# Performance work log

Hardware: AMD Instinct MI355X
Metric: run time of the kernel (lower is better)

## Reference

```python
import jax, jax.numpy as jnp
import numpy as np

B, T, C, H = 2, 2048, 1024, 16
DH = C // H
EPS = 1e-5


def _rotary(t_len, d_head):
    inv_freq = 1.0 / (10000.0 ** (jnp.arange(0, d_head, 2, dtype=jnp.float32) / d_head))
    t = jnp.arange(t_len, dtype=jnp.float32)
    freqs = t[:, None] * inv_freq[None, :]           # [T, dh/2]
    emb = jnp.concatenate([freqs, freqs], axis=-1)    # [T, dh]
    return jnp.cos(emb), jnp.sin(emb)


def _apply_rope(x, cos, sin):
    # x: [B,H,T,dh]; cos/sin: [T,dh]
    d = x.shape[-1]
    x1, x2 = x[..., : d // 2], x[..., d // 2 :]
    x_rot = jnp.concatenate([-x2, x1], axis=-1)
    return x * cos + x_rot * sin


def _decay_mask(t_len, n_head):
    gammas = 1.0 - 2.0 ** (-5.0 - jnp.arange(n_head, dtype=jnp.float32))  # [H]
    n = jnp.arange(t_len)[:, None]
    m = jnp.arange(t_len)[None, :]
    dist = n - m
    decay = gammas[:, None, None] ** jnp.maximum(dist, 0).astype(jnp.float32)
    return jnp.where(dist[None] >= 0, decay, 0.0)  # [H,T,T]


def setup_inputs() -> dict:
    key = jax.random.key(0)
    ks = jax.random.split(key, 7)
    s = 1.0 / np.sqrt(C)
    return {
        "x": jax.random.normal(ks[0], (B, T, C), dtype=jnp.float32),
        "Wq": jax.random.normal(ks[1], (C, C), dtype=jnp.float32) * s,
        "Wk": jax.random.normal(ks[2], (C, C), dtype=jnp.float32) * s,
        "Wv": jax.random.normal(ks[3], (C, C), dtype=jnp.float32) * s,
        "Wo": jax.random.normal(ks[4], (C, C), dtype=jnp.float32) * s,
        "gn_weight": jnp.ones((C,), dtype=jnp.float32),
        "gn_bias": jnp.zeros((C,), dtype=jnp.float32),
    }


def reference(x, Wq, Wk, Wv, Wo, gn_weight, gn_bias):
    b, t, c = x.shape
    # projections (torch Linear: y = x @ W.T), split heads -> [B,H,T,dh]
    def proj(W):
        return jnp.einsum("btc,oc->bto", x, W).reshape(b, t, H, DH).transpose(0, 2, 1, 3)
    q, k, v = proj(Wq), proj(Wk), proj(Wv)

    cos, sin = _rotary(t, DH)
    q = _apply_rope(q, cos, sin)
    k = _apply_rope(k, cos, sin)

    decay = _decay_mask(t, H)                          # [H,T,T]
    qk = jnp.einsum("bhtd,bhsd->bhts", q, k) * (1.0 / np.sqrt(DH))
    qk = qk * decay[None]
    out = jnp.einsum("bhts,bhsd->bhtd", qk, v)         # [B,H,T,dh]

    # GroupNorm with n_head groups over channels, per token
    out = out.transpose(0, 2, 1, 3)                    # [B,T,H,dh]
    mu = jnp.mean(out, axis=-1, keepdims=True)
    var = jnp.mean((out - mu) ** 2, axis=-1, keepdims=True)
    out = (out - mu) * jax.lax.rsqrt(var + EPS)
    out = out * gn_weight.reshape(H, DH) + gn_bias.reshape(H, DH)

    out = out.reshape(b, t, c)
    return jnp.einsum("btc,oc->bto", out, Wo)
```

## Files before the change

kernel.cpp:

```cpp
#include <hip/hip_runtime.h>
#include <stdint.h>

#define B_ 2
#define T_ 2048
#define C_ 1024
#define H_ 16
#define DH_ 64
#define M_ (B_*T_)

typedef short bhalf8 __attribute__((ext_vector_type(8)));
typedef float floatx4 __attribute__((ext_vector_type(4)));

__device__ __forceinline__ short f2bf(float f) {
  unsigned u = __float_as_uint(f);
  u += 0x7fffu + ((u >> 16) & 1u);
  return (short)(u >> 16);
}
__device__ __forceinline__ float bf2f(short s) {
  return __uint_as_float(((unsigned)(unsigned short)s) << 16);
}

__device__ __forceinline__ void gll16(void* lds_dst, const void* g_src) {
  __builtin_amdgcn_global_load_lds(
      reinterpret_cast<const uint32_t __attribute__((address_space(1)))*>(
          reinterpret_cast<uintptr_t>(g_src)),
      reinterpret_cast<uint32_t __attribute__((address_space(3)))*>(
          reinterpret_cast<uintptr_t>(lds_dst)),
      16, 0, 0);
}

__global__ void cvt_all(
    const float* __restrict__ x,  const float* __restrict__ wq,
    const float* __restrict__ wk, const float* __restrict__ wv,
    const float* __restrict__ wo,
    short* __restrict__ xb, short* __restrict__ wqb, short* __restrict__ wkb,
    short* __restrict__ wvb, short* __restrict__ wob)
{
  int i = blockIdx.x * blockDim.x + threadIdx.x;
  const float* s; short* d; int off;
  if (i < (M_*C_/4)) { s = x; d = xb; off = i; }
  else {
    int j = i - M_*C_/4;
    int w = j >> 18;
    off = j & ((1<<18) - 1);
    s = (w==0) ? wq : (w==1) ? wk : (w==2) ? wv : wo;
    d = (w==0) ? wqb : (w==1) ? wkb : (w==2) ? wvb : wob;
  }
  float4 v = ((const float4*)s)[off];
  short4 o;
  o.x = f2bf(v.x); o.y = f2bf(v.y); o.z = f2bf(v.z); o.w = f2bf(v.w);
  ((short4*)d)[off] = o;
}

__global__ __launch_bounds__(256) void gemm_qkv(
    const short* __restrict__ X,
    const short* __restrict__ Wq, const short* __restrict__ Wk, const short* __restrict__ Wv,
    short* __restrict__ Qb, short* __restrict__ Kb, short* __restrict__ Vt)
{
  __shared__ __align__(16) short As[128*64];
  __shared__ __align__(16) short Bs[128*64];
  const int tid  = threadIdx.x;
  const int lane = tid & 63;
  const int wv   = tid >> 6;
  const int l15  = lane & 15;
  const int quad = lane >> 4;
  const int wm   = (wv >> 1) << 6;
  const int wn   = (wv & 1) << 6;
  const int nx   = blockIdx.x;
  const int m0   = blockIdx.y << 7;
  const int K    = C_;

  const short *Ab, *Bb;
  int nloc, kind;
  if (nx < 8)       { kind = 0; nloc = nx << 7;        Ab = X  + (size_t)m0*K;   Bb = Wq + (size_t)nloc*K; }
  else if (nx < 16) { kind = 1; nloc = (nx - 8) << 7;  Ab = X  + (size_t)m0*K;   Bb = Wk + (size_t)nloc*K; }
  else              { kind = 2; nloc = (nx - 16) << 7; Ab = Wv + (size_t)nloc*K; Bb = X  + (size_t)m0*K;   }

  floatx4 acc[4][4] = {};

  for (int k0 = 0; k0 < K; k0 += 64) {
    __syncthreads();
#pragma unroll
    for (int i = 0; i < 4; ++i) {
      int c = (i<<8) + tid, r = c >> 3, g = (c & 7) ^ (r & 7);
      gll16(&As[((i<<8) + (wv<<6))*8], Ab + (size_t)r*K + k0 + (g<<3));
      gll16(&Bs[((i<<8) + (wv<<6))*8], Bb + (size_t)r*K + k0 + (g<<3));
    }
    __syncthreads();
#pragma unroll
    for (int ks = 0; ks < 2; ++ks) {
      bhalf8 af[4], bfr[4];
#pragma unroll
      for (int rt = 0; rt < 4; ++rt) {
        int row = wm + rt*16 + l15;
        af[rt] = *(const bhalf8*)&As[(row<<6) + ((((ks<<2)+quad) ^ (row&7))<<3)];
      }
#pragma unroll
      for (int ct = 0; ct < 4; ++ct) {
        int row = wn + ct*16 + l15;
        bfr[ct] = *(const bhalf8*)&Bs[(row<<6) + ((((ks<<2)+quad) ^ (row&7))<<3)];
      }
#pragma unroll
      for (int rt = 0; rt < 4; ++rt)
#pragma unroll
        for (int ct = 0; ct < 4; ++ct)
          acc[rt][ct] = __builtin_amdgcn_mfma_f32_16x16x32_bf16(af[rt], bfr[ct], acc[rt][ct], 0, 0, 0);
    }
  }

  if (kind < 2) {
    short* Cb = kind ? Kb : Qb;
    const int hh = (nloc + wn) >> 6;
#pragma unroll
    for (int rt = 0; rt < 4; ++rt)
#pragma unroll
      for (int r = 0; r < 4; ++r) {
        int n  = m0 + wm + rt*16 + quad*4 + r;
        int bb = n >> 11, t = n & (T_-1);
        size_t base = ((size_t)(bb*H_ + hh)*T_ + t)*DH_;
        float tf = (float)t;
#pragma unroll
        for (int ct = 0; ct < 2; ++ct) {
          int ii = ct*16 + l15;
          float ang = tf * exp2f((float)ii * (-0.4152410118609203f));
          float sn = __sinf(ang), cs = __cosf(ang);
          float xlo = acc[rt][ct][r], xhi = acc[rt][ct+2][r];
          Cb[base + ii]      = f2bf(xlo*cs - xhi*sn);
          Cb[base + ii + 32] = f2bf(xhi*cs + xlo*sn);
        }
      }
  } else {
#pragma unroll
    for (int rt = 0; rt < 4; ++rt)
#pragma unroll
      for (int r = 0; r < 4; ++r) {
        int o = nloc + wm + rt*16 + quad*4 + r;
#pragma unroll
        for (int ct = 0; ct < 4; ++ct) {
          int n  = m0 + wn + ct*16 + l15;
          int bb = n >> 11, t = n & (T_-1);
          Vt[(size_t)bb*(C_*T_) + (size_t)o*T_ + t] = f2bf(acc[rt][ct][r]);
        }
      }
  }
}

__global__ __launch_bounds__(256) void gemm_out(
    const short* __restrict__ A, const short* __restrict__ Bm, float* __restrict__ Cf)
{
  __shared__ __align__(16) short As[128*64];
  __shared__ __align__(16) short Bs[64*64];
  const int tid = threadIdx.x, lane = tid & 63, wv = tid >> 6;
  const int l15 = lane & 15, quad = lane >> 4;
  const int n0 = blockIdx.x << 6;
  const int m0 = blockIdx.y << 7;

  floatx4 acc[2][4] = {};
  const short* Ab = A  + (size_t)m0 * C_;
  const short* Bb = Bm + (size_t)n0 * C_;

  for (int k0 = 0; k0 < C_; k0 += 64) {
    __syncthreads();
#pragma unroll
    for (int i = 0; i < 4; ++i) {
      int c = (i<<8) + tid, r = c >> 3, g = (c & 7) ^ (r & 7);
      gll16(&As[((i<<8) + (wv<<6))*8], Ab + (size_t)r*C_ + k0 + (g<<3));
    }
#pragma unroll
    for (int i = 0; i < 2; ++i) {
      int c = (i<<8) + tid, r = c >> 3, g = (c & 7) ^ (r & 7);
      gll16(&Bs[((i<<8) + (wv<<6))*8], Bb + (size_t)r*C_ + k0 + (g<<3));
    }
    __syncthreads();
#pragma unroll
    for (int ks = 0; ks < 2; ++ks) {
      bhalf8 af[2], bfr[4];
#pragma unroll
      for (int rt = 0; rt < 2; ++rt) {
        int row = (wv<<5) + rt*16 + l15;
        af[rt] = *(const bhalf8*)&As[(row<<6) + ((((ks<<2)+quad) ^ (row&7))<<3)];
      }
#pragma unroll
      for (int ct = 0; ct < 4; ++ct) {
        int row = ct*16 + l15;
        bfr[ct] = *(const bhalf8*)&Bs[(row<<6) + ((((ks<<2)+quad) ^ (row&7))<<3)];
      }
#pragma unroll
      for (int rt = 0; rt < 2; ++rt)
#pragma unroll
        for (int ct = 0; ct < 4; ++ct)
          acc[rt][ct] = __builtin_amdgcn_mfma_f32_16x16x32_bf16(af[rt], bfr[ct], acc[rt][ct], 0, 0, 0);
    }
  }

#pragma unroll
  for (int rt = 0; rt < 2; ++rt)
#pragma unroll
    for (int r = 0; r < 4; ++r) {
      int n = m0 + (wv<<5) + rt*16 + quad*4 + r;
#pragma unroll
      for (int ct = 0; ct < 4; ++ct)
        Cf[(size_t)n * C_ + n0 + ct*16 + l15] = acc[rt][ct][r];
    }
}

__global__ __launch_bounds__(256) void transpose_k(
    const short* __restrict__ Kb, short* __restrict__ Kt)
{
  __shared__ short tile[64*66];
  const int idx = blockIdx.x, bh = idx >> 5, tc = idx & 31;
  const int t0 = tc << 6;
  const short* src = Kb + ((size_t)bh*T_ + t0) * DH_;
  int row = threadIdx.x >> 2, c0 = (threadIdx.x & 3) << 4;
  *(int4*)&tile[row*66 + c0]     = *(const int4*)&src[row*64 + c0];
  *(int4*)&tile[row*66 + c0 + 8] = *(const int4*)&src[row*64 + c0 + 8];
  __syncthreads();
  short* dst = Kt + (size_t)bh*DH_*T_;
  int d = threadIdx.x >> 2, k0 = (threadIdx.x & 3) << 4;
  short tmp[16];
#pragma unroll
  for (int i = 0; i < 16; ++i) tmp[i] = tile[(k0 + i)*66 + d];
  *(int4*)&dst[(size_t)d*T_ + t0 + k0]     = *(const int4*)&tmp[0];
  *(int4*)&dst[(size_t)d*T_ + t0 + k0 + 8] = *(const int4*)&tmp[8];
}

__global__ __launch_bounds__(256) void seg_state(
    const short* __restrict__ Kt, const short* __restrict__ Vt,
    short* __restrict__ Pseg)
{
  __shared__ __align__(16) short Ks[64*64];
  __shared__ __align__(16) short Vs[64*64];
  const int tid = threadIdx.x, lane = tid & 63, wv = tid >> 6;
  const int l15 = lane & 15, quad = lane >> 4;
  const int wrow = wv << 4;
  const int bh = blockIdx.x >> 2, p = blockIdx.x & 3;
  const int h = bh & 15;
  const float log2g = log2f(1.f - exp2f(-5.f - (float)h));
  const float g64 = exp2f(log2g * 64.f);

  float wgt[16];
#pragma unroll
  for (int ks = 0; ks < 2; ++ks)
#pragma unroll
    for (int i = 0; i < 8; ++i)
      wgt[ks*8 + i] = exp2f(log2g * (float)(64 - (ks*32 + (quad<<3) + i)));

  const short* Ktg = Kt + (size_t)bh*DH_*T_;
  const short* Vtg = Vt + (size_t)bh*DH_*T_;

  floatx4 acc[4] = {};
  for (int j = 0; j < 8; ++j) {
    const int m0 = ((p<<3) + j) << 6;
    __syncthreads();
#pragma unroll
    for (int i = 0; i < 2; ++i) {
      int slot = (i<<8) + tid;
      int r = slot >> 3, g = (slot & 7) ^ (r & 7);
      gll16(&Ks[((i<<8) + (wv<<6))*8], Ktg + (size_t)r*T_ + m0 + (g<<3));
      gll16(&Vs[((i<<8) + (wv<<6))*8], Vtg + (size_t)r*T_ + m0 + (g<<3));
    }
    __syncthreads();
#pragma unroll
    for (int ct = 0; ct < 4; ++ct)
#pragma unroll
      for (int r = 0; r < 4; ++r) acc[ct][r] *= g64;
#pragma unroll
    for (int ks = 0; ks < 2; ++ks) {
      int row = wrow + l15;
      bhalf8 va = *(const bhalf8*)&Vs[(row<<6) + ((((ks<<2)+quad) ^ (row&7))<<3)];
      bhalf8 aw;
#pragma unroll
      for (int i = 0; i < 8; ++i) aw[i] = f2bf(bf2f(va[i]) * wgt[ks*8 + i]);
      bhalf8 bk[4];
#pragma unroll
      for (int ct = 0; ct < 4; ++ct) {
        int kr = ct*16 + l15;
        bk[ct] = *(const bhalf8*)&Ks[(kr<<6) + ((((ks<<2)+quad) ^ (kr&7))<<3)];
      }
#pragma unroll
      for (int ct = 0; ct < 4; ++ct)
        acc[ct] = __builtin_amdgcn_mfma_f32_16x16x32_bf16(aw, bk[ct], acc[ct], 0, 0, 0);
    }
  }
  size_t base = (size_t)(bh*4 + p) * 2 * 4096;
#pragma unroll
  for (int ct = 0; ct < 4; ++ct)
#pragma unroll
    for (int r = 0; r < 4; ++r) {
      int e = wrow + (quad<<2) + r, d = ct*16 + l15;
      float x = acc[ct][r];
      short hi = f2bf(x);
      short lo = f2bf(x - bf2f(hi));
      Pseg[base + e*64 + d]        = hi;
      Pseg[base + 4096 + e*64 + d] = lo;
    }
}

__global__ __launch_bounds__(256) void retention_chunk(
    const short* __restrict__ Qb, const short* __restrict__ Kb,
    const short* __restrict__ Kt, const short* __restrict__ Vt,
    const short* __restrict__ Pseg,
    const float* __restrict__ gnw, const float* __restrict__ gnb,
    short* __restrict__ Xn)
{
  __shared__ __align__(16) short Vs[64*64];
  __shared__ __align__(16) short Kts[64*64];
  __shared__ __align__(16) short KSs[64*64];
  __shared__ __align__(16) short Sh[64*64];
  __shared__ __align__(16) short Sl[64*64];

  const int tid = threadIdx.x, lane = tid & 63, wv = tid >> 6;
  const int l15 = lane & 15, quad = lane >> 4;
  const int wrow = wv << 4;

  const int idx = blockIdx.x;
  const int bh = idx & 31;
  const int cc = idx >> 5;
  const int c  = ((cc & 7) << 2) | (cc >> 3);
  const int p = c >> 3, j = c & 7;
  const int b = bh >> 4, h = bh & 15;
  const int n0 = c << 6;

  const float log2g = log2f(1.f - exp2f(-5.f - (float)h));
  const float g64 = exp2f(log2g * 64.f);

  const short* Qg  = Qb + ((size_t)bh*T_ + n0 + wrow) * DH_;
  const short* Kg  = Kb + (size_t)bh*T_*DH_;
  const short* Ktg = Kt + (size_t)bh*DH_*T_;
  const short* Vtg = Vt + (size_t)bh*DH_*T_;

  bhalf8 aq[2];
#pragma unroll
  for (int ks = 0; ks < 2; ++ks)
    aq[ks] = *(const bhalf8*)(Qg + (size_t)l15*DH_ + ks*32 + quad*8);

  float rowf[4], colf0[4];
#pragma unroll
  for (int r = 0; r < 4; ++r)
    rowf[r] = exp2f(log2g * (float)(wrow + (quad<<2) + r)) * 0.125f;
#pragma unroll
  for (int ct = 0; ct < 4; ++ct)
    colf0[ct] = exp2f(-log2g * (float)(ct*16 + l15));

  const bool has_state = (c > 0);

  floatx4 st[4] = {};
  if (j > 0) {
    float wgt[16];
#pragma unroll
    for (int ks = 0; ks < 2; ++ks)
#pragma unroll
      for (int i = 0; i < 8; ++i)
        wgt[ks*8 + i] = exp2f(log2g * (float)(64 - (ks*32 + (quad<<3) + i)));
    for (int jp = 0; jp < j; ++jp) {
      if (log2g * (float)((j - 1 - jp) << 6) < -34.f) continue;
      const int m0 = ((p<<3) + jp) << 6;
      __syncthreads();
#pragma unroll
      for (int i = 0; i < 2; ++i) {
        int slot = (i<<8) + tid;
        int r = slot >> 3, g = (slot & 7) ^ (r & 7);
        gll16(&Kts[((i<<8) + (wv<<6))*8], Ktg + (size_t)r*T_ + m0 + (g<<3));
        gll16(&Vs[((i<<8) + (wv<<6))*8],  Vtg + (size_t)r*T_ + m0 + (g<<3));
      }
      __syncthreads();
#pragma unroll
      for (int ct = 0; ct < 4; ++ct)
#pragma unroll
        for (int r = 0; r < 4; ++r) st[ct][r] *= g64;
#pragma unroll
      for (int ks = 0; ks < 2; ++ks) {
        int row = wrow + l15;
        bhalf8 va = *(const bhalf8*)&Vs[(row<<6) + ((((ks<<2)+quad) ^ (row&7))<<3)];
        bhalf8 aw;
#pragma unroll
        for (int i = 0; i < 8; ++i) aw[i] = f2bf(bf2f(va[i]) * wgt[ks*8 + i]);
        bhalf8 bk[4];
#pragma unroll
        for (int ct = 0; ct < 4; ++ct) {
          int kr = ct*16 + l15;
          bk[ct] = *(const bhalf8*)&Kts[(kr<<6) + ((((ks<<2)+quad) ^ (kr&7))<<3)];
        }
#pragma unroll
        for (int ct = 0; ct < 4; ++ct)
          st[ct] = __builtin_amdgcn_mfma_f32_16x16x32_bf16(aw, bk[ct], st[ct], 0, 0, 0);
      }
    }
  }
  for (int pp = 0; pp < p; ++pp) {
    float wexp = log2g * (float)(n0 - ((pp + 1) << 9));
    if (wexp < -34.f) continue;
    float w = exp2f(wexp);
    const short* Pg = Pseg + (size_t)(bh*4 + pp) * 2 * 4096;
#pragma unroll
    for (int ct = 0; ct < 4; ++ct)
#pragma unroll
      for (int r = 0; r < 4; ++r) {
        int e = wrow + (quad<<2) + r, d = ct*16 + l15;
        st[ct][r] += w * (bf2f(Pg[e*64 + d]) + bf2f(Pg[4096 + e*64 + d]));
      }
  }
  if (has_state) {
#pragma unroll
    for (int ct = 0; ct < 4; ++ct)
#pragma unroll
      for (int r = 0; r < 4; ++r) {
        int e = wrow + (quad<<2) + r, d = ct*16 + l15;
        float x = st[ct][r];
        short hi = f2bf(x);
        short lo = f2bf(x - bf2f(hi));
        int addr = (e<<6) + ((((d>>3) ^ (e&7))<<3)) + (d&7);
        Sh[addr] = hi; Sl[addr] = lo;
      }
  }

  __syncthreads();
#pragma unroll
  for (int i = 0; i < 2; ++i) {
    int slot = (i<<8) + tid;
    int r = slot >> 3, g = (slot & 7) ^ (r & 7);
    gll16(&KSs[((i<<8) + (wv<<6))*8], Kg  + (size_t)(n0 + r)*DH_ + (g<<3));
    gll16(&Vs[((i<<8) + (wv<<6))*8],  Vtg + (size_t)r*T_ + n0 + (g<<3));
  }
  __syncthreads();

  floatx4 sacc[4] = {};
#pragma unroll
  for (int ks = 0; ks < 2; ++ks) {
    bhalf8 bk[4];
#pragma unroll
    for (int ct = 0; ct < 4; ++ct) {
      int row = ct*16 + l15;
      bk[ct] = *(const bhalf8*)&KSs[(row<<6) + ((((ks<<2)+quad) ^ (row&7))<<3)];
    }
#pragma unroll
    for (int ct = 0; ct < 4; ++ct)
      sacc[ct] = __builtin_amdgcn_mfma_f32_16x16x32_bf16(aq[ks], bk[ct], sacc[ct], 0, 0, 0);
  }
  __syncthreads();
#pragma unroll
  for (int ct = 0; ct < 4; ++ct) {
    float cf = colf0[ct];
    int colg = (ct<<1) + (l15>>3);
    int m = ct*16 + l15;
#pragma unroll
    for (int r = 0; r < 4; ++r) {
      int row = wrow + (quad<<2) + r;
      float v = (row >= m) ? sacc[ct][r] * (rowf[r] * cf) : 0.f;
      KSs[(row<<6) + ((colg ^ ((row>>1)&7))<<3) + (l15&7)] = f2bf(v);
    }
  }
  floatx4 oacc[4] = {};
#pragma unroll
  for (int ks = 0; ks < 2; ++ks) {
    int row = wrow + l15;
    bhalf8 as_ = *(const bhalf8*)&KSs[(row<<6) + ((((ks<<2)+quad) ^ ((row>>1)&7))<<3)];
    bhalf8 bv[4];
#pragma unroll
    for (int ct = 0; ct < 4; ++ct) {
      int vrow = ct*16 + l15;
      bv[ct] = *(const bhalf8*)&Vs[(vrow<<6) + ((((ks<<2)+quad) ^ (vrow&7))<<3)];
    }
#pragma unroll
    for (int ct = 0; ct < 4; ++ct)
      oacc[ct] = __builtin_amdgcn_mfma_f32_16x16x32_bf16(as_, bv[ct], oacc[ct], 0, 0, 0);
  }

  if (has_state) {
    floatx4 iacc[4] = {};
#pragma unroll
    for (int ks = 0; ks < 2; ++ks) {
      bhalf8 bhf[4], blf[4];
#pragma unroll
      for (int ct = 0; ct < 4; ++ct) {
        int er = ct*16 + l15;
        int ga = ((((ks<<2)+quad) ^ (er&7))<<3);
        bhf[ct] = *(const bhalf8*)&Sh[(er<<6) + ga];
        blf[ct] = *(const bhalf8*)&Sl[(er<<6) + ga];
      }
#pragma unroll
      for (int ct = 0; ct < 4; ++ct) {
        iacc[ct] = __builtin_amdgcn_mfma_f32_16x16x32_bf16(aq[ks], bhf[ct], iacc[ct], 0, 0, 0);
        iacc[ct] = __builtin_amdgcn_mfma_f32_16x16x32_bf16(aq[ks], blf[ct], iacc[ct], 0, 0, 0);
      }
    }
#pragma unroll
    for (int ct = 0; ct < 4; ++ct)
#pragma unroll
      for (int r = 0; r < 4; ++r)
        oacc[ct][r] += rowf[r] * iacc[ct][r];
  }

#pragma unroll
  for (int r = 0; r < 4; ++r) {
    float s1 = oacc[0][r] + oacc[1][r] + oacc[2][r] + oacc[3][r];
    float s2 = oacc[0][r]*oacc[0][r] + oacc[1][r]*oacc[1][r]
             + oacc[2][r]*oacc[2][r] + oacc[3][r]*oacc[3][r];
#pragma unroll
    for (int off = 1; off < 16; off <<= 1) {
      s1 += __shfl_xor(s1, off);
      s2 += __shfl_xor(s2, off);
    }
    float mean = s1 * (1.f/64.f);
    float var  = s2 * (1.f/64.f) - mean*mean;
    float rstd = rsqrtf(var + 1e-5f);
    int t = n0 + wrow + (quad<<2) + r;
    size_t obase = ((size_t)b*T_ + t)*C_ + h*DH_;
#pragma unroll
    for (int ct = 0; ct < 4; ++ct) {
      int d = ct*16 + l15;
      float y = (oacc[ct][r] - mean)*rstd*gnw[h*DH_ + d] + gnb[h*DH_ + d];
      Xn[obase + d] = f2bf(y);
    }
  }
}

extern "C" void kernel_launch(void* const* d_in, const int* in_sizes, int n_in,
                              void* d_out, int out_size, void* d_ws, size_t ws_size,
                              hipStream_t stream) {
  (void)in_sizes; (void)n_in; (void)out_size; (void)ws_size;
  const float* x   = (const float*)d_in[0];
  const float* Wq  = (const float*)d_in[1];
  const float* Wk  = (const float*)d_in[2];
  const float* Wv  = (const float*)d_in[3];
  const float* Wo  = (const float*)d_in[4];
  const float* gnw = (const float*)d_in[5];
  const float* gnb = (const float*)d_in[6];
  float* out = (float*)d_out;

  char* ws = (char*)d_ws;
  short* Xb   = (short*)(ws);
  short* Ktb  = (short*)(ws);
  short* Wqb  = (short*)(ws + (8u<<20));
  short* Pseg = (short*)(ws + (8u<<20));
  short* Wkb  = (short*)(ws + (10u<<20));
  short* Wvb  = (short*)(ws + (12u<<20));
  short* Wob  = (short*)(ws + (14u<<20));
  short* Qb   = (short*)(ws + (16u<<20));
  short* Kb   = (short*)(ws + (24u<<20));
  short* Vtw  = (short*)(ws + (32u<<20));
  short* Xn   = (short*)(ws + (40u<<20));

  cvt_all<<<(M_*C_/4 + 4*(C_*C_/4)) / 256, 256, 0, stream>>>(
      x, Wq, Wk, Wv, Wo, Xb, Wqb, Wkb, Wvb, Wob);

  gemm_qkv<<<dim3(24, 32), 256, 0, stream>>>(Xb, Wqb, Wkb, Wvb, Qb, Kb, Vtw);
  transpose_k<<<1024, 256, 0, stream>>>(Kb, Ktb);
  seg_state<<<128, 256, 0, stream>>>(Ktb, Vtw, Pseg);
  retention_chunk<<<1024, 256, 0, stream>>>(Qb, Kb, Ktb, Vtw, Pseg, gnw, gnb, Xn);
  gemm_out<<<dim3(16, 32), 256, 0, stream>>>(Xn, Wob, out);
}
```

Measured before the change: 183.6 us.

## Double-buffer GEMM and segment-state LDS loads; split segments into eight parts

Both GEMMs now use a 32-wide K slice with two LDS buffers, so the next slice's global-to-LDS load is issued before the MFMAs on the current slice. This removes one barrier per iteration and hides load latency. seg_state also double-buffers, and the segment count per head grows from 4 to 8, giving 256 blocks instead of 128. retention_chunk adds one more cross-segment state term per chunk in exchange for shorter intra-segment loops.

```diff
diff --git a/kernel.cpp b/kernel.cpp
--- a/kernel.cpp
+++ b/kernel.cpp
@@ -57,8 +57,8 @@
     const short* __restrict__ Wq, const short* __restrict__ Wk, const short* __restrict__ Wv,
     short* __restrict__ Qb, short* __restrict__ Kb, short* __restrict__ Vt)
 {
-  __shared__ __align__(16) short As[128*64];
-  __shared__ __align__(16) short Bs[128*64];
+  __shared__ __align__(16) short As[2][128*32];
+  __shared__ __align__(16) short Bs[2][128*32];
   const int tid  = threadIdx.x;
   const int lane = tid & 63;
   const int wv   = tid >> 6;
@@ -76,36 +76,39 @@
   else if (nx < 16) { kind = 1; nloc = (nx - 8) << 7;  Ab = X  + (size_t)m0*K;   Bb = Wk + (size_t)nloc*K; }
   else              { kind = 2; nloc = (nx - 16) << 7; Ab = Wv + (size_t)nloc*K; Bb = X  + (size_t)m0*K;   }
 
+  auto stage = [&](int buf, int k0) {
+#pragma unroll
+    for (int i = 0; i < 2; ++i) {
+      int pA = (i<<8) + tid;
+      int r = pA >> 2, go = (pA & 3) ^ ((r >> 1) & 3);
+      gll16(&As[buf][((i<<8) + (wv<<6))*8], Ab + (size_t)r*K + k0 + (go<<3));
+      gll16(&Bs[buf][((i<<8) + (wv<<6))*8], Bb + (size_t)r*K + k0 + (go<<3));
+    }
+  };
+
   floatx4 acc[4][4] = {};
-
-  for (int k0 = 0; k0 < K; k0 += 64) {
+  stage(0, 0);
+  int cur = 0;
+  for (int it = 0; it < 32; ++it) {
     __syncthreads();
-#pragma unroll
-    for (int i = 0; i < 4; ++i) {
-      int c = (i<<8) + tid, r = c >> 3, g = (c & 7) ^ (r & 7);
-      gll16(&As[((i<<8) + (wv<<6))*8], Ab + (size_t)r*K + k0 + (g<<3));
-      gll16(&Bs[((i<<8) + (wv<<6))*8], Bb + (size_t)r*K + k0 + (g<<3));
-    }
-    __syncthreads();
-#pragma unroll
-    for (int ks = 0; ks < 2; ++ks) {
-      bhalf8 af[4], bfr[4];
-#pragma unroll
-      for (int rt = 0; rt < 4; ++rt) {
-        int row = wm + rt*16 + l15;
-        af[rt] = *(const bhalf8*)&As[(row<<6) + ((((ks<<2)+quad) ^ (row&7))<<3)];
-      }
-#pragma unroll
-      for (int ct = 0; ct < 4; ++ct) {
-        int row = wn + ct*16 + l15;
-        bfr[ct] = *(const bhalf8*)&Bs[(row<<6) + ((((ks<<2)+quad) ^ (row&7))<<3)];
-      }
-#pragma unroll
-      for (int rt = 0; rt < 4; ++rt)
-#pragma unroll
-        for (int ct = 0; ct < 4; ++ct)
-          acc[rt][ct] = __builtin_amdgcn_mfma_f32_16x16x32_bf16(af[rt], bfr[ct], acc[rt][ct], 0, 0, 0);
-    }
+    if (it < 31) stage(cur ^ 1, (it + 1) << 5);
+    bhalf8 af[4], bfr[4];
+#pragma unroll
+    for (int rt = 0; rt < 4; ++rt) {
+      int row = wm + rt*16 + l15;
+      af[rt] = *(const bhalf8*)&As[cur][(row<<5) + ((quad ^ ((row>>1)&3))<<3)];
+    }
+#pragma unroll
+    for (int ct = 0; ct < 4; ++ct) {
+      int row = wn + ct*16 + l15;
+      bfr[ct] = *(const bhalf8*)&Bs[cur][(row<<5) + ((quad ^ ((row>>1)&3))<<3)];
+    }
+#pragma unroll
+    for (int rt = 0; rt < 4; ++rt)
+#pragma unroll
+      for (int ct = 0; ct < 4; ++ct)
+        acc[rt][ct] = __builtin_amdgcn_mfma_f32_16x16x32_bf16(af[rt], bfr[ct], acc[rt][ct], 0, 0, 0);
+    cur ^= 1;
   }
 
   if (kind < 2) {
@@ -148,49 +151,51 @@
 __global__ __launch_bounds__(256) void gemm_out(
     const short* __restrict__ A, const short* __restrict__ Bm, float* __restrict__ Cf)
 {
-  __shared__ __align__(16) short As[128*64];
-  __shared__ __align__(16) short Bs[64*64];
+  __shared__ __align__(16) short As[2][128*32];
+  __shared__ __align__(16) short Bs[2][64*32];
   const int tid = threadIdx.x, lane = tid & 63, wv = tid >> 6;
   const int l15 = lane & 15, quad = lane >> 4;
   const int n0 = blockIdx.x << 6;
   const int m0 = blockIdx.y << 7;
 
-  floatx4 acc[2][4] = {};
   const short* Ab = A  + (size_t)m0 * C_;
   const short* Bb = Bm + (size_t)n0 * C_;
 
-  for (int k0 = 0; k0 < C_; k0 += 64) {
+  auto stage = [&](int buf, int k0) {
+#pragma unroll
+    for (int i = 0; i < 2; ++i) {
+      int p = (i<<8) + tid, r = p >> 2, go = (p & 3) ^ ((r >> 1) & 3);
+      gll16(&As[buf][((i<<8) + (wv<<6))*8], Ab + (size_t)r*C_ + k0 + (go<<3));
+    }
+    {
+      int p = tid, r = p >> 2, go = (p & 3) ^ ((r >> 1) & 3);
+      gll16(&Bs[buf][(wv<<6)*8], Bb + (size_t)r*C_ + k0 + (go<<3));
+    }
+  };
+
+  floatx4 acc[2][4] = {};
+  stage(0, 0);
+  int cur = 0;
+  for (int it = 0; it < 32; ++it) {
     __syncthreads();
-#pragma unroll
-    for (int i = 0; i < 4; ++i) {
-      int c = (i<<8) + tid, r = c >> 3, g = (c & 7) ^ (r & 7);
-      gll16(&As[((i<<8) + (wv<<6))*8], Ab + (size_t)r*C_ + k0 + (g<<3));
-    }
-#pragma unroll
-    for (int i = 0; i < 2; ++i) {
-      int c = (i<<8) + tid, r = c >> 3, g = (c & 7) ^ (r & 7);
-      gll16(&Bs[((i<<8) + (wv<<6))*8], Bb + (size_t)r*C_ + k0 + (g<<3));
-    }
-    __syncthreads();
-#pragma unroll
-    for (int ks = 0; ks < 2; ++ks) {
-      bhalf8 af[2], bfr[4];
-#pragma unroll
-      for (int rt = 0; rt < 2; ++rt) {
-        int row = (wv<<5) + rt*16 + l15;
-        af[rt] = *(const bhalf8*)&As[(row<<6) + ((((ks<<2)+quad) ^ (row&7))<<3)];
-      }
-#pragma unroll
-      for (int ct = 0; ct < 4; ++ct) {
-        int row = ct*16 + l15;
-        bfr[ct] = *(const bhalf8*)&Bs[(row<<6) + ((((ks<<2)+quad) ^ (row&7))<<3)];
-      }
-#pragma unroll
-      for (int rt = 0; rt < 2; ++rt)
-#pragma unroll
-        for (int ct = 0; ct < 4; ++ct)
-          acc[rt][ct] = __builtin_amdgcn_mfma_f32_16x16x32_bf16(af[rt], bfr[ct], acc[rt][ct], 0, 0, 0);
-    }
+    if (it < 31) stage(cur ^ 1, (it + 1) << 5);
+    bhalf8 af[2], bfr[4];
+#pragma unroll
+    for (int rt = 0; rt < 2; ++rt) {
+      int row = (wv<<5) + rt*16 + l15;
+      af[rt] = *(const bhalf8*)&As[cur][(row<<5) + ((quad ^ ((row>>1)&3))<<3)];
+    }
+#pragma unroll
+    for (int ct = 0; ct < 4; ++ct) {
+      int row = ct*16 + l15;
+      bfr[ct] = *(const bhalf8*)&Bs[cur][(row<<5) + ((quad ^ ((row>>1)&3))<<3)];
+    }
+#pragma unroll
+    for (int rt = 0; rt < 2; ++rt)
+#pragma unroll
+      for (int ct = 0; ct < 4; ++ct)
+        acc[rt][ct] = __builtin_amdgcn_mfma_f32_16x16x32_bf16(af[rt], bfr[ct], acc[rt][ct], 0, 0, 0);
+    cur ^= 1;
   }
 
 #pragma unroll
@@ -228,12 +233,12 @@
     const short* __restrict__ Kt, const short* __restrict__ Vt,
     short* __restrict__ Pseg)
 {
-  __shared__ __align__(16) short Ks[64*64];
-  __shared__ __align__(16) short Vs[64*64];
+  __shared__ __align__(16) short Ks[2][64*64];
+  __shared__ __align__(16) short Vs[2][64*64];
   const int tid = threadIdx.x, lane = tid & 63, wv = tid >> 6;
   const int l15 = lane & 15, quad = lane >> 4;
   const int wrow = wv << 4;
-  const int bh = blockIdx.x >> 2, p = blockIdx.x & 3;
+  const int bh = blockIdx.x >> 3, p = blockIdx.x & 7;
   const int h = bh & 15;
   const float log2g = log2f(1.f - exp2f(-5.f - (float)h));
   const float g64 = exp2f(log2g * 64.f);
@@ -248,18 +253,23 @@
   const short* Ktg = Kt + (size_t)bh*DH_*T_;
   const short* Vtg = Vt + (size_t)bh*DH_*T_;
 
-  floatx4 acc[4] = {};
-  for (int j = 0; j < 8; ++j) {
-    const int m0 = ((p<<3) + j) << 6;
-    __syncthreads();
+  auto stage = [&](int buf, int jc) {
+    const int m0 = ((p<<2) + jc) << 6;
 #pragma unroll
     for (int i = 0; i < 2; ++i) {
       int slot = (i<<8) + tid;
       int r = slot >> 3, g = (slot & 7) ^ (r & 7);
-      gll16(&Ks[((i<<8) + (wv<<6))*8], Ktg + (size_t)r*T_ + m0 + (g<<3));
-      gll16(&Vs[((i<<8) + (wv<<6))*8], Vtg + (size_t)r*T_ + m0 + (g<<3));
-    }
+      gll16(&Ks[buf][((i<<8) + (wv<<6))*8], Ktg + (size_t)r*T_ + m0 + (g<<3));
+      gll16(&Vs[buf][((i<<8) + (wv<<6))*8], Vtg + (size_t)r*T_ + m0 + (g<<3));
+    }
+  };
+
+  floatx4 acc[4] = {};
+  stage(0, 0);
+  int cur = 0;
+  for (int j = 0; j < 4; ++j) {
     __syncthreads();
+    if (j < 3) stage(cur ^ 1, j + 1);
 #pragma unroll
     for (int ct = 0; ct < 4; ++ct)
 #pragma unroll
@@ -267,7 +277,7 @@
 #pragma unroll
     for (int ks = 0; ks < 2; ++ks) {
       int row = wrow + l15;
-      bhalf8 va = *(const bhalf8*)&Vs[(row<<6) + ((((ks<<2)+quad) ^ (row&7))<<3)];
+      bhalf8 va = *(const bhalf8*)&Vs[cur][(row<<6) + ((((ks<<2)+quad) ^ (row&7))<<3)];
       bhalf8 aw;
 #pragma unroll
       for (int i = 0; i < 8; ++i) aw[i] = f2bf(bf2f(va[i]) * wgt[ks*8 + i]);
@@ -275,14 +285,15 @@
 #pragma unroll
       for (int ct = 0; ct < 4; ++ct) {
         int kr = ct*16 + l15;
-        bk[ct] = *(const bhalf8*)&Ks[(kr<<6) + ((((ks<<2)+quad) ^ (kr&7))<<3)];
+        bk[ct] = *(const bhalf8*)&Ks[cur][(kr<<6) + ((((ks<<2)+quad) ^ (kr&7))<<3)];
       }
 #pragma unroll
       for (int ct = 0; ct < 4; ++ct)
         acc[ct] = __builtin_amdgcn_mfma_f32_16x16x32_bf16(aw, bk[ct], acc[ct], 0, 0, 0);
     }
-  }
-  size_t base = (size_t)(bh*4 + p) * 2 * 4096;
+    cur ^= 1;
+  }
+  size_t base = (size_t)(bh*8 + p) * 2 * 4096;
 #pragma unroll
   for (int ct = 0; ct < 4; ++ct)
 #pragma unroll
@@ -317,7 +328,7 @@
   const int bh = idx & 31;
   const int cc = idx >> 5;
   const int c  = ((cc & 7) << 2) | (cc >> 3);
-  const int p = c >> 3, j = c & 7;
+  const int p = c >> 2, j = c & 3;
   const int b = bh >> 4, h = bh & 15;
   const int n0 = c << 6;
 
@@ -354,7 +365,7 @@
         wgt[ks*8 + i] = exp2f(log2g * (float)(64 - (ks*32 + (quad<<3) + i)));
     for (int jp = 0; jp < j; ++jp) {
       if (log2g * (float)((j - 1 - jp) << 6) < -34.f) continue;
-      const int m0 = ((p<<3) + jp) << 6;
+      const int m0 = ((p<<2) + jp) << 6;
       __syncthreads();
 #pragma unroll
       for (int i = 0; i < 2; ++i) {
@@ -388,10 +399,10 @@
     }
   }
   for (int pp = 0; pp < p; ++pp) {
-    float wexp = log2g * (float)(n0 - ((pp + 1) << 9));
+    float wexp = log2g * (float)(n0 - ((pp + 1) << 8));
     if (wexp < -34.f) continue;
     float w = exp2f(wexp);
-    const short* Pg = Pseg + (size_t)(bh*4 + pp) * 2 * 4096;
+    const short* Pg = Pseg + (size_t)(bh*8 + pp) * 2 * 4096;
 #pragma unroll
     for (int ct = 0; ct < 4; ++ct)
 #pragma unroll
@@ -546,7 +557,7 @@
 
   gemm_qkv<<<dim3(24, 32), 256, 0, stream>>>(Xb, Wqb, Wkb, Wvb, Qb, Kb, Vtw);
   transpose_k<<<1024, 256, 0, stream>>>(Kb, Ktb);
-  seg_state<<<128, 256, 0, stream>>>(Ktb, Vtw, Pseg);
+  seg_state<<<256, 256, 0, stream>>>(Ktb, Vtw, Pseg);
   retention_chunk<<<1024, 256, 0, stream>>>(Qb, Kb, Ktb, Vtw, Pseg, gnw, gnb, Xn);
   gemm_out<<<dim3(16, 32), 256, 0, stream>>>(Xn, Wob, out);
 }
```

After: 174.1 us. -5.2%, faster.
